# Kernel optimization log

Measured on AMD Instinct MI355X. Metric: run time of the kernel, lower is better.

Reference implementation:

```python
import jax, jax.numpy as jnp
import numpy as np

D_MODEL = 1024

def setup_inputs() -> dict:
    key = jax.random.key(0)
    ks = jax.random.split(key, 9)
    s = 1.0 / np.sqrt(D_MODEL)
    x = jax.random.normal(ks[0], (4, 2048, D_MODEL), dtype=jnp.float32)
    Wq = jax.random.uniform(ks[1], (D_MODEL, D_MODEL), jnp.float32, -s, s)
    bq = jax.random.uniform(ks[2], (D_MODEL,), jnp.float32, -s, s)
    Wk = jax.random.uniform(ks[3], (D_MODEL, D_MODEL), jnp.float32, -s, s)
    bk = jax.random.uniform(ks[4], (D_MODEL,), jnp.float32, -s, s)
    Wv = jax.random.uniform(ks[5], (D_MODEL, D_MODEL), jnp.float32, -s, s)
    bv = jax.random.uniform(ks[6], (D_MODEL,), jnp.float32, -s, s)
    Wo = jax.random.uniform(ks[7], (D_MODEL, D_MODEL), jnp.float32, -s, s)
    bo = jax.random.uniform(ks[8], (D_MODEL,), jnp.float32, -s, s)
    return {"x": x, "Wq": Wq, "bq": bq, "Wk": Wk, "bk": bk,
            "Wv": Wv, "bv": bv, "Wo": Wo, "bo": bo}

def reference(x, Wq, bq, Wk, bk, Wv, bv, Wo, bo):
    # Linear projections (weights stored as [in, out])
    q = x @ Wq + bq  # [b, s, d]
    k = x @ Wk + bk
    v = x @ Wv + bv
    d_k = q.shape[-1]
    scores = jnp.einsum("bqd,bkd->bqk", q, k) / jnp.sqrt(jnp.float32(d_k))
    p = jax.nn.softmax(scores, axis=-1)
    attn = jnp.einsum("bqk,bkd->bqd", p, v)
    return attn @ Wo + bo
```

## Files before the change

### kernel.cpp

```cpp
#include <hip/hip_runtime.h>
#include <stdint.h>

#define D_MODEL 1024
#define SEQ 2048
#define NBATCH 4

typedef __attribute__((ext_vector_type(4))) float f32x4;
typedef __attribute__((ext_vector_type(8))) __bf16 bf16x8;
typedef __attribute__((ext_vector_type(4))) unsigned short u16x4;

__device__ __forceinline__ float b2f(unsigned short u) {
    union { unsigned int i; float f; } c; c.i = ((unsigned int)u) << 16; return c.f;
}
__device__ __forceinline__ unsigned short f2b(float f) {
    union { float f; unsigned int i; } c; c.f = f;
    unsigned int u = c.i;
    u += 0x7FFFu + ((u >> 16) & 1u);
    return (unsigned short)(u >> 16);
}

__device__ __forceinline__ void glds16(void* lds, const void* g) {
    __builtin_amdgcn_global_load_lds((const __attribute__((address_space(1))) void*)g,
                                     (__attribute__((address_space(3))) void*)lds,
                                     16, 0, 0);
}

__device__ __forceinline__ void xcd_map(int& xx, int& yy, int& zz)
{
    const int gx = gridDim.x, gy = gridDim.y;
    int bid = blockIdx.x + gx * (blockIdx.y + gy * blockIdx.z);
    const int H = gy >> 3;
    const int xcd = bid & 7;
    int slot = bid >> 3;
    yy = xcd * H + (slot % H);
    slot /= H;
    xx = slot % gx;
    zz = slot / gx;
}

__device__ __forceinline__ void gemm_tile(const unsigned short* __restrict__ A,
                                          const unsigned short* __restrict__ Bt,
                                          int K, int m0, int n0,
                                          f32x4 (&acc)[4][4])
{
    __shared__ alignas(16) unsigned short As[128 * 64];
    __shared__ alignas(16) unsigned short Bs[128 * 64];

    const int t    = threadIdx.x;
    const int wave = t >> 6;
    const int lane = t & 63;
    const int srow = t >> 3;
    const int sch  = ((t & 7) ^ (srow & 7)) * 8;

    const unsigned short* Ag = A  + (long)(m0 + srow) * K + sch;
    const unsigned short* Bg = Bt + (long)(n0 + srow) * K + sch;

    char* AsB = (char*)As + wave * 1024;
    char* BsB = (char*)Bs + wave * 1024;

    const int wm   = (wave >> 1) * 64;
    const int wn   = (wave & 1) * 64;
    const int fr   = lane & 15;
    const int quad = lane >> 4;
    const int rp0  = ((quad    ) ^ (fr & 7)) * 16;
    const int rp1  = ((4 + quad) ^ (fr & 7)) * 16;

    for (int k0 = 0; k0 < K; k0 += 64) {
        __syncthreads();
        #pragma unroll
        for (int j = 0; j < 4; ++j) {
            glds16(AsB + j * 4096, Ag + (long)(j * 32) * K + k0);
            glds16(BsB + j * 4096, Bg + (long)(j * 32) * K + k0);
        }
        __syncthreads();

        #pragma unroll
        for (int s = 0; s < 2; ++s) {
            const int ro = s ? rp1 : rp0;
            bf16x8 af[4], bfv[4];
            #pragma unroll
            for (int i = 0; i < 4; ++i)
                af[i] = *(const bf16x8*)((const char*)As + (wm + i * 16 + fr) * 128 + ro);
            #pragma unroll
            for (int i = 0; i < 4; ++i)
                bfv[i] = *(const bf16x8*)((const char*)Bs + (wn + i * 16 + fr) * 128 + ro);

            #pragma unroll
            for (int mi = 0; mi < 4; ++mi)
                #pragma unroll
                for (int ni = 0; ni < 4; ++ni)
                    acc[mi][ni] = __builtin_amdgcn_mfma_f32_16x16x32_bf16(
                                      af[mi], bfv[ni], acc[mi][ni], 0, 0, 0);
        }
    }
}

template<bool BIAS, typename OutT>
__global__ __launch_bounds__(256)
void gemm_bt(const unsigned short* __restrict__ A,
             const unsigned short* __restrict__ Bt,
             const float* __restrict__ bias,
             OutT* __restrict__ C,
             int N, int K, long sA, long sB, long sC)
{
    int xx, yy, zz;
    xcd_map(xx, yy, zz);
    A  += (long)zz * sA;
    Bt += (long)zz * sB;
    C  += (long)zz * sC;
    const int m0 = yy * 128;
    const int n0 = xx * 128;

    f32x4 acc[4][4] = {};
    gemm_tile(A, Bt, K, m0, n0, acc);

    const int t = threadIdx.x, wave = t >> 6, lane = t & 63;
    const int wm = (wave >> 1) * 64, wn = (wave & 1) * 64;
    const int fr = lane & 15, quad = lane >> 4;

    float bb[4] = {0.f, 0.f, 0.f, 0.f};
    if (BIAS) {
        #pragma unroll
        for (int ni = 0; ni < 4; ++ni)
            bb[ni] = bias[n0 + wn + ni * 16 + fr];
    }

    #pragma unroll
    for (int mi = 0; mi < 4; ++mi) {
        const int rowb = m0 + wm + mi * 16 + quad * 4;
        #pragma unroll
        for (int ni = 0; ni < 4; ++ni) {
            const int col = n0 + wn + ni * 16 + fr;
            f32x4 v = acc[mi][ni];
            if constexpr (sizeof(OutT) == 4) {
                #pragma unroll
                for (int r = 0; r < 4; ++r)
                    C[(long)(rowb + r) * N + col] = v[r] + bb[ni];
            } else {
                #pragma unroll
                for (int r = 0; r < 4; ++r)
                    C[(long)(rowb + r) * N + col] = (OutT)f2b(v[r] + bb[ni]);
            }
        }
    }
}

__global__ __launch_bounds__(256)
void qkv_gemm(const unsigned short* __restrict__ xb,
              const unsigned short* __restrict__ Wqt,
              const unsigned short* __restrict__ Wkt,
              const unsigned short* __restrict__ Wvt,
              const float* __restrict__ bq, const float* __restrict__ bk,
              const float* __restrict__ bv,
              unsigned short* __restrict__ Q, unsigned short* __restrict__ Kb,
              unsigned short* __restrict__ Vt)
{
    int xx, yy, zz;
    xcd_map(xx, yy, zz);

    const unsigned short* Bt; const float* bias; unsigned short* C; bool tstore = false;
    switch (zz) {
        case 0:  Bt = Wqt; bias = bq; C = Q;  break;
        case 1:  Bt = Wkt; bias = bk; C = Kb; break;
        default: Bt = Wvt; bias = bv; C = Vt; tstore = true; break;
    }
    const int m0 = yy * 128;
    const int n0 = xx * 128;
    const int N = D_MODEL, K = D_MODEL;

    f32x4 acc[4][4] = {};
    gemm_tile(xb, Bt, K, m0, n0, acc);

    const int t = threadIdx.x, wave = t >> 6, lane = t & 63;
    const int wm = (wave >> 1) * 64, wn = (wave & 1) * 64;
    const int fr = lane & 15, quad = lane >> 4;

    float bb[4];
    #pragma unroll
    for (int ni = 0; ni < 4; ++ni)
        bb[ni] = bias[n0 + wn + ni * 16 + fr];

    #pragma unroll
    for (int mi = 0; mi < 4; ++mi) {
        const int rowb = m0 + wm + mi * 16 + quad * 4;
        #pragma unroll
        for (int ni = 0; ni < 4; ++ni) {
            const int col = n0 + wn + ni * 16 + fr;
            f32x4 v = acc[mi][ni];
            if (!tstore) {
                #pragma unroll
                for (int r = 0; r < 4; ++r)
                    C[(long)(rowb + r) * N + col] = f2b(v[r] + bb[ni]);
            } else {
                u16x4 pk;
                #pragma unroll
                for (int r = 0; r < 4; ++r)
                    pk[r] = f2b(v[r] + bb[ni]);
                unsigned short* dst = C + ((long)(rowb >> 11)) * ((long)N * SEQ)
                                        + (long)col * SEQ + (rowb & (SEQ - 1));
                *(u16x4*)dst = pk;
            }
        }
    }
}

__global__ __launch_bounds__(256)
void softmax_inplace(unsigned short* __restrict__ S)
{
    const long row = blockIdx.x;
    unsigned short* s = S + row * SEQ;
    const int t = threadIdx.x;

    u16x4 a = ((const u16x4*)s)[t];
    u16x4 b = ((const u16x4*)s)[t + 256];
    float v[8];
    #pragma unroll
    for (int i = 0; i < 4; ++i) { v[i] = b2f(a[i]); v[4 + i] = b2f(b[i]); }

    float mx = v[0];
    #pragma unroll
    for (int i = 1; i < 8; ++i) mx = fmaxf(mx, v[i]);
    #pragma unroll
    for (int off = 32; off; off >>= 1) mx = fmaxf(mx, __shfl_xor(mx, off));

    __shared__ float red[8];
    const int wv = t >> 6, ln = t & 63;
    if (ln == 0) red[wv] = mx;
    __syncthreads();
    mx = fmaxf(fmaxf(red[0], red[1]), fmaxf(red[2], red[3]));

    const float sc = 0.03125f;
    float e[8], sum = 0.f;
    #pragma unroll
    for (int i = 0; i < 8; ++i) { e[i] = __expf((v[i] - mx) * sc); sum += e[i]; }
    #pragma unroll
    for (int off = 32; off; off >>= 1) sum += __shfl_xor(sum, off);
    if (ln == 0) red[4 + wv] = sum;
    __syncthreads();
    sum = (red[4] + red[5]) + (red[6] + red[7]);
    const float inv = 1.f / sum;

    u16x4 o;
    #pragma unroll
    for (int i = 0; i < 4; ++i) o[i] = f2b(e[i] * inv);
    ((u16x4*)s)[t] = o;
    #pragma unroll
    for (int i = 0; i < 4; ++i) o[i] = f2b(e[4 + i] * inv);
    ((u16x4*)s)[t + 256] = o;
}

__global__ __launch_bounds__(256)
void prep(const float* __restrict__ x, unsigned short* __restrict__ xb,
          const float* __restrict__ W0, const float* __restrict__ W1,
          const float* __restrict__ W2, const float* __restrict__ W3,
          unsigned short* __restrict__ T0, unsigned short* __restrict__ T1,
          unsigned short* __restrict__ T2, unsigned short* __restrict__ T3)
{
    const int bid = blockIdx.x;
    if (bid < 8192) {
        long i = ((long)bid * 256 + threadIdx.x) * 4;
        f32x4 v = *(const f32x4*)(x + i);
        u16x4 o;
        #pragma unroll
        for (int r = 0; r < 4; ++r) o[r] = f2b(v[r]);
        *(u16x4*)(xb + i) = o;
        return;
    }
    const int b2 = bid - 8192;
    const float* W; unsigned short* T;
    switch (b2 >> 10) {
        case 0:  W = W0; T = T0; break;
        case 1:  W = W1; T = T1; break;
        case 2:  W = W2; T = T2; break;
        default: W = W3; T = T3; break;
    }
    const int tile = b2 & 1023;
    const int bx = (tile & 31) * 32, by = (tile >> 5) * 32;
    __shared__ float buf[32][33];
    const int tx = threadIdx.x & 31, ty = threadIdx.x >> 5;
    #pragma unroll
    for (int i = 0; i < 32; i += 8)
        buf[ty + i][tx] = W[(long)(by + ty + i) * D_MODEL + bx + tx];
    __syncthreads();
    #pragma unroll
    for (int i = 0; i < 32; i += 8)
        T[(long)(bx + ty + i) * D_MODEL + by + tx] = f2b(buf[tx][ty + i]);
}

extern "C" void kernel_launch(void* const* d_in, const int* in_sizes, int n_in,
                              void* d_out, int out_size, void* d_ws, size_t ws_size,
                              hipStream_t stream)
{
    const float* x  = (const float*)d_in[0];
    const float* Wq = (const float*)d_in[1];
    const float* bq = (const float*)d_in[2];
    const float* Wk = (const float*)d_in[3];
    const float* bk = (const float*)d_in[4];
    const float* Wv = (const float*)d_in[5];
    const float* bv = (const float*)d_in[6];
    const float* Wo = (const float*)d_in[7];
    const float* bo = (const float*)d_in[8];
    float* out = (float*)d_out;

    char* ws = (char*)d_ws;
    const size_t MB = 1024ull * 1024ull;
    unsigned short* Wqt = (unsigned short*)(ws + 0 * MB);
    unsigned short* Wkt = (unsigned short*)(ws + 2 * MB);
    unsigned short* Wvt = (unsigned short*)(ws + 4 * MB);
    unsigned short* Wot = (unsigned short*)(ws + 6 * MB);
    unsigned short* xb  = (unsigned short*)(ws + 8 * MB);
    unsigned short* Q   = (unsigned short*)(ws + 24 * MB);
    unsigned short* Kb  = (unsigned short*)(ws + 40 * MB);
    unsigned short* Vt  = (unsigned short*)(ws + 56 * MB);
    unsigned short* At  = (unsigned short*)(ws + 72 * MB);
    unsigned short* S   = (unsigned short*)(ws + 88 * MB);

    const dim3 blk(256);

    prep<<<dim3(12288), blk, 0, stream>>>(x, xb, Wq, Wk, Wv, Wo, Wqt, Wkt, Wvt, Wot);

    qkv_gemm<<<dim3(8, 64, 3), blk, 0, stream>>>(xb, Wqt, Wkt, Wvt, bq, bk, bv, Q, Kb, Vt);

    gemm_bt<false, unsigned short><<<dim3(16, 16, 4), blk, 0, stream>>>(
        Q, Kb, nullptr, S, 2048, 1024,
        (long)2048 * 1024, (long)2048 * 1024, (long)2048 * 2048);

    softmax_inplace<<<dim3(NBATCH * SEQ), blk, 0, stream>>>(S);

    gemm_bt<false, unsigned short><<<dim3(8, 16, 4), blk, 0, stream>>>(
        S, Vt, nullptr, At, 1024, 2048,
        (long)2048 * 2048, (long)1024 * 2048, (long)2048 * 1024);

    gemm_bt<true, float><<<dim3(8, 64, 1), blk, 0, stream>>>(
        At, Wot, bo, out, 1024, 1024, 0, 0, 0);
}
```

Baseline: 307.0 us.

## Double-buffer GEMM LDS tiles with BK=32 to overlap loads and MFMA

Restructures the shared GEMM tile loop into a two-stage pipeline. Each stage uses a 32-wide K slice, and the next slice is loaded asynchronously into the alternate LDS buffer while MFMAs run on the current one. This cuts the two barriers per iteration down to one and hides global-to-LDS latency, with a new swizzle for the narrower rows. In exchange there are twice as many iterations with fewer MFMAs each, so loop and barrier overhead per FLOP goes up.

After: 314.1 us. 1.02x slower.

```diff
diff --git a/kernel.cpp b/kernel.cpp
--- a/kernel.cpp
+++ b/kernel.cpp
@@ -43,55 +43,62 @@
                                           int K, int m0, int n0,
                                           f32x4 (&acc)[4][4])
 {
-    __shared__ alignas(16) unsigned short As[128 * 64];
-    __shared__ alignas(16) unsigned short Bs[128 * 64];
+    __shared__ alignas(16) unsigned short As[2 * 128 * 32];
+    __shared__ alignas(16) unsigned short Bs[2 * 128 * 32];
 
     const int t    = threadIdx.x;
     const int wave = t >> 6;
     const int lane = t & 63;
-    const int srow = t >> 3;
-    const int sch  = ((t & 7) ^ (srow & 7)) * 8;
+
+    const int srow = (wave << 4) + (lane >> 2);
+    const int sch  = ((lane & 3) ^ ((srow >> 1) & 3)) * 8;
 
     const unsigned short* Ag = A  + (long)(m0 + srow) * K + sch;
     const unsigned short* Bg = Bt + (long)(n0 + srow) * K + sch;
 
-    char* AsB = (char*)As + wave * 1024;
-    char* BsB = (char*)Bs + wave * 1024;
-
-    const int wm   = (wave >> 1) * 64;
-    const int wn   = (wave & 1) * 64;
-    const int fr   = lane & 15;
-    const int quad = lane >> 4;
-    const int rp0  = ((quad    ) ^ (fr & 7)) * 16;
-    const int rp1  = ((4 + quad) ^ (fr & 7)) * 16;
-
-    for (int k0 = 0; k0 < K; k0 += 64) {
+    char* AsW = (char*)As + wave * 1024;
+    char* BsW = (char*)Bs + wave * 1024;
+
+    const int fr = lane & 15, quad = lane >> 4;
+    const int wm = (wave >> 1) * 64, wn = (wave & 1) * 64;
+    const int slot = (quad ^ ((fr >> 1) & 3)) * 16;
+    const int aoff = (wm + fr) * 64 + slot;
+    const int boff = (wn + fr) * 64 + slot;
+
+    auto stage = [&](int buf, int ko) {
+        #pragma unroll
+        for (int j = 0; j < 2; ++j) {
+            glds16(AsW + buf * 8192 + j * 4096, Ag + (long)(j * 64) * K + ko);
+            glds16(BsW + buf * 8192 + j * 4096, Bg + (long)(j * 64) * K + ko);
+        }
+    };
+
+    stage(0, 0);
+    __syncthreads();
+
+    int buf = 0;
+    for (int k0 = 0; k0 < K; k0 += 32) {
+        if (k0 + 32 < K) stage(buf ^ 1, k0 + 32);
+
+        const char* Ab = (const char*)As + buf * 8192;
+        const char* Bb = (const char*)Bs + buf * 8192;
+        bf16x8 af[4], bv[4];
+        #pragma unroll
+        for (int i = 0; i < 4; ++i)
+            af[i] = *(const bf16x8*)(Ab + aoff + i * 1024);
+        #pragma unroll
+        for (int i = 0; i < 4; ++i)
+            bv[i] = *(const bf16x8*)(Bb + boff + i * 1024);
+
+        #pragma unroll
+        for (int mi = 0; mi < 4; ++mi)
+            #pragma unroll
+            for (int ni = 0; ni < 4; ++ni)
+                acc[mi][ni] = __builtin_amdgcn_mfma_f32_16x16x32_bf16(
+                                  af[mi], bv[ni], acc[mi][ni], 0, 0, 0);
+
         __syncthreads();
-        #pragma unroll
-        for (int j = 0; j < 4; ++j) {
-            glds16(AsB + j * 4096, Ag + (long)(j * 32) * K + k0);
-            glds16(BsB + j * 4096, Bg + (long)(j * 32) * K + k0);
-        }
-        __syncthreads();
-
-        #pragma unroll
-        for (int s = 0; s < 2; ++s) {
-            const int ro = s ? rp1 : rp0;
-            bf16x8 af[4], bfv[4];
-            #pragma unroll
-            for (int i = 0; i < 4; ++i)
-                af[i] = *(const bf16x8*)((const char*)As + (wm + i * 16 + fr) * 128 + ro);
-            #pragma unroll
-            for (int i = 0; i < 4; ++i)
-                bfv[i] = *(const bf16x8*)((const char*)Bs + (wn + i * 16 + fr) * 128 + ro);
-
-            #pragma unroll
-            for (int mi = 0; mi < 4; ++mi)
-                #pragma unroll
-                for (int ni = 0; ni < 4; ++ni)
-                    acc[mi][ni] = __builtin_amdgcn_mfma_f32_16x16x32_bf16(
-                                      af[mi], bfv[ni], acc[mi][ni], 0, 0, 0);
-        }
+        buf ^= 1;
     }
 }
 
```
